# Kernel optimization log

Measured on AMD Instinct MI355X. Metric: run time of the kernel, lower is better.

Reference implementation:

```python
import jax, jax.numpy as jnp
import numpy as np

B, C, H, W = 512, 128, 16, 16
WS, HALO, HEADS = 16, 4, 4
HD = C // HEADS            # 32
SCALE = HD ** -0.5
WSH = WS + 2 * HALO        # 24 (padded window size)


def setup_inputs() -> dict:
    key = jax.random.key(0)
    ks = jax.random.split(key, 5)
    return {
        "x": jax.random.normal(ks[0], (B, C, H, W), dtype=jnp.float32),
        "qkv_w": jax.random.normal(ks[1], (3 * C, C), dtype=jnp.float32) * 0.02,
        "qkv_b": jax.random.normal(ks[2], (3 * C,), dtype=jnp.float32) * 0.02,
        "proj_w": jax.random.normal(ks[3], (C, C), dtype=jnp.float32) * 0.02,
        "proj_b": jax.random.normal(ks[4], (C,), dtype=jnp.float32) * 0.02,
    }


def reference(x, qkv_w, qkv_b, proj_w, proj_b):
    b, c, h, w = x.shape
    # reflect pad spatial dims by HALO
    xp = jnp.pad(x, ((0, 0), (0, 0), (HALO, HALO), (HALO, HALO)), mode="reflect")
    hp, wp = h + 2 * HALO, w + 2 * HALO
    # window partition on BHWC with window size WSH (non-overlapping, as in source)
    xw = xp.transpose(0, 2, 3, 1)  # [B, Hp, Wp, C]
    nh, nw = hp // WSH, wp // WSH
    xw = xw.reshape(b, nh, WSH, nw, WSH, c).transpose(0, 1, 3, 2, 4, 5)
    xw = xw.reshape(-1, WSH * WSH, c)  # [nW, 576, C]
    # QKV
    qkv = xw @ qkv_w.T + qkv_b  # [nW, 576, 3C]
    qkv = qkv.reshape(-1, WSH * WSH, 3, HEADS, HD).transpose(2, 0, 3, 1, 4)
    q, k, v = qkv[0], qkv[1], qkv[2]  # [nW, heads, 576, HD]
    # center query slice (contiguous flat slice, faithful to source)
    cs = HALO * WSH + HALO
    csz = WS * WS
    qc = jax.lax.dynamic_slice_in_dim(q, cs, csz, axis=2)  # [nW, heads, 256, HD]
    attn = jax.nn.softmax(jnp.einsum("whqd,whkd->whqk", qc, k) * SCALE, axis=-1)
    out = jnp.einsum("whqk,whkd->wqhd", attn, v).reshape(-1, csz, c)
    out = out @ proj_w.T + proj_b  # [nW, 256, C]
    # window reverse with window size WS over original H, W
    out = out.reshape(b, h // WS, w // WS, WS, WS, c).transpose(0, 1, 3, 2, 4, 5)
    out = out.reshape(b, h, w, c)
    return out.transpose(0, 3, 1, 2)  # [B, C, H, W]
```

## Files before the change

kernel.cpp:

```cpp
#include <hip/hip_runtime.h>
#include <hip/hip_bf16.h>
#include <stdint.h>


typedef short bf16x8 __attribute__((ext_vector_type(8)));
typedef float f32x4 __attribute__((ext_vector_type(4)));

__device__ __forceinline__ unsigned short f2bf(float f) {
  unsigned int u = __builtin_bit_cast(unsigned int, f);
  u += 0x7fffu + ((u >> 16) & 1u);
  return (unsigned short)(u >> 16);
}

__device__ __forceinline__ unsigned int cvt_pk_bf16(float lo, float hi) {
  unsigned int r;
  asm("v_cvt_pk_bf16_f32 %0, %1, %2" : "=v"(r) : "v"(lo), "v"(hi));
  return r;
}

__device__ __forceinline__ f32x4 mfma_16x16x32(bf16x8 a, bf16x8 b, f32x4 c) {
  return __builtin_amdgcn_mfma_f32_16x16x32_bf16(a, b, c, 0, 0, 0);
}

__device__ __forceinline__ void bar_lds() {
  asm volatile("s_waitcnt lgkmcnt(0)\n\ts_barrier" ::: "memory");
}

__global__ void wcvt(const float* __restrict__ proj_w, unsigned short* __restrict__ wp) {
  int i = blockIdx.x * 256 + threadIdx.x;
  if (i < 16384) wp[i] = f2bf(proj_w[i]);
}

__global__ __launch_bounds__(256, 2) void qkv_kernel(
    const float* __restrict__ x, const float* __restrict__ qkv_w,
    const float* __restrict__ qkv_b, unsigned short* __restrict__ qc,
    unsigned short* __restrict__ kw, unsigned short* __restrict__ vw) {
  __shared__ __align__(16) unsigned int XS[256 * 64];
  __shared__ __align__(16) unsigned short OB[64 * 128];
  const int b = blockIdx.x;
  const int tid = threadIdx.x;
  const int lane = tid & 63;
  const int wid = tid >> 6;
  const int g = lane >> 4;
  const int r16 = lane & 15;

  const float* xb = x + (size_t)b * 32768;

  bf16x8 wfr[6][4];
  float bias[6];
  #pragma unroll
  for (int i = 0; i < 6; ++i) {
    int nt_abs = wid + 4 * i;
    int n = nt_abs * 16 + r16;
    bias[i] = qkv_b[n];
    #pragma unroll
    for (int kt = 0; kt < 4; ++kt) {
      const float* wsrc = qkv_w + n * 128 + kt * 32 + g * 8;
      float4 w0 = *(const float4*)wsrc;
      float4 w1 = *(const float4*)(wsrc + 4);
      bf16x8 f;
      f[0] = (short)f2bf(w0.x); f[1] = (short)f2bf(w0.y);
      f[2] = (short)f2bf(w0.z); f[3] = (short)f2bf(w0.w);
      f[4] = (short)f2bf(w1.x); f[5] = (short)f2bf(w1.y);
      f[6] = (short)f2bf(w1.z); f[7] = (short)f2bf(w1.w);
      wfr[i][kt] = f;
    }
  }

  #pragma unroll 4
  for (int it = 0; it < 64; ++it) {
    float f0 = xb[(2 * it) * 256 + tid];
    float f1 = xb[(2 * it + 1) * 256 + tid];
    unsigned int pk = (unsigned int)f2bf(f0) | ((unsigned int)f2bf(f1) << 16);
    XS[tid * 64 + (it ^ ((tid & 7) << 2))] = pk;
  }
  bar_lds();

  for (int tile = 0; tile < 9; ++tile) {
    int sv[4];
    #pragma unroll
    for (int mt = 0; mt < 4; ++mt) {
      int tg = tile * 64 + mt * 16 + r16;
      int ph = tg / 24;
      int pw = tg - ph * 24;
      int hh = ph - 4; hh = (hh < 0) ? -hh : ((hh > 15) ? 30 - hh : hh);
      int wc = pw - 4; wc = (wc < 0) ? -wc : ((wc > 15) ? 30 - wc : wc);
      sv[mt] = hh * 16 + wc;
    }

    f32x4 acc[6][4];
    #pragma unroll
    for (int i = 0; i < 6; ++i)
      #pragma unroll
      for (int mt = 0; mt < 4; ++mt) acc[i][mt] = f32x4{0.f, 0.f, 0.f, 0.f};

    #pragma unroll
    for (int kt = 0; kt < 4; ++kt) {
      bf16x8 afr[4];
      #pragma unroll
      for (int mt = 0; mt < 4; ++mt)
        afr[mt] = __builtin_bit_cast(
            bf16x8, *(const uint4*)&XS[sv[mt] * 64 + ((kt * 16 + g * 4) ^ ((sv[mt] & 7) << 2))]);
      #pragma unroll
      for (int i = 0; i < 6; ++i)
        #pragma unroll
        for (int mt = 0; mt < 4; ++mt)
          acc[i][mt] = mfma_16x16x32(afr[mt], wfr[i][kt], acc[i][mt]);
    }

    #pragma unroll
    for (int sel = 0; sel < 3; ++sel) {
      bar_lds();
      #pragma unroll
      for (int j = 0; j < 2; ++j) {
        const int i = sel * 2 + j;
        int dcol = (wid + 4 * j) * 16 + r16;
        #pragma unroll
        for (int mt = 0; mt < 4; ++mt)
          #pragma unroll
          for (int rr = 0; rr < 4; ++rr)
            OB[(mt * 16 + 4 * g + rr) * 128 + dcol] = f2bf(acc[i][mt][rr] + bias[i]);
      }
      bar_lds();
      #pragma unroll
      for (int it = 0; it < 4; ++it) {
        int flat = it * 2048 + tid * 8;
        int tokl = flat >> 7, d0 = flat & 127;
        int tg = tile * 64 + tokl;
        uint4 val = *(const uint4*)&OB[tokl * 128 + d0];
        if (sel == 0) {
          int qi = tg - 100;
          if ((unsigned)qi < 256u)
            *(uint4*)(qc + ((size_t)b * 256 + qi) * 128 + d0) = val;
        } else if (sel == 1) {
          *(uint4*)(kw + ((size_t)b * 576 + tg) * 128 + d0) = val;
        } else {
          *(uint4*)(vw + ((size_t)b * 576 + tg) * 128 + d0) = val;
        }
      }
    }
  }
}

__global__ __launch_bounds__(256) void attn_kernel(
    const unsigned short* __restrict__ qc, const unsigned short* __restrict__ kw,
    const unsigned short* __restrict__ vw, unsigned short* __restrict__ ao) {
  __shared__ __align__(16) unsigned int KF[4 * 192 * 4];
  __shared__ __align__(16) unsigned short VT[32 * 200];
  const int bh = blockIdx.x;
  const int tid = threadIdx.x;
  const int lane = tid & 63;
  const int wid = tid >> 6;
  const int g = lane >> 4;
  const int r16 = lane & 15;
  const int qb = wid * 64;
  const int b = bh >> 2, h = bh & 3;

  const unsigned short* qcb = qc + (size_t)b * 256 * 128 + h * 32;
  const unsigned short* kb = kw + (size_t)b * 576 * 128 + h * 32;
  const unsigned short* vb = vw + (size_t)b * 576 * 128 + h * 32;

  unsigned int kreg[12], vreg[12];
  {
    const unsigned int* ks = (const unsigned int*)kb;
    const unsigned int* vs = (const unsigned int*)vb;
    #pragma unroll
    for (int it = 0; it < 12; ++it) {
      int f = it * 256 + tid;
      int kv = f >> 4, cu = f & 15;
      kreg[it] = ks[kv * 64 + cu];
      vreg[it] = vs[kv * 64 + cu];
    }
  }

  bf16x8 qf[4];
  #pragma unroll
  for (int qnt = 0; qnt < 4; ++qnt)
    qf[qnt] = __builtin_bit_cast(bf16x8, *(const uint4*)(qcb + (size_t)(qb + qnt * 16 + r16) * 128 + g * 8));

  float ls[4];
  #pragma unroll
  for (int i = 0; i < 4; ++i) ls[i] = 0.f;
  f32x4 oa[2][4];
  #pragma unroll
  for (int i = 0; i < 2; ++i)
    #pragma unroll
    for (int j = 0; j < 4; ++j) oa[i][j] = f32x4{0.f, 0.f, 0.f, 0.f};

  const float KE = 0.17677669529663687f * 1.4426950408889634f;

  for (int ch = 0; ch < 3; ++ch) {
    if (ch) bar_lds();
    #pragma unroll
    for (int it = 0; it < 12; ++it) {
      int f = it * 256 + tid;
      int kv = f >> 4, cu = f & 15;
      KF[(cu >> 2) * 768 + kv * 4 + (cu & 3)] = kreg[it];
      int kv32 = kv & 31;
      int idx = (kv >> 5) * 32 + ((kv32 & 15) >> 2) * 8 + (kv32 >> 4) * 4 + (kv32 & 3);
      unsigned int pk = vreg[it];
      VT[(2 * cu) * 200 + idx] = (unsigned short)(pk & 0xffffu);
      VT[(2 * cu + 1) * 200 + idx] = (unsigned short)(pk >> 16);
    }
    bar_lds();
    if (ch < 2) {
      const unsigned int* ks = (const unsigned int*)(kb + (size_t)(ch + 1) * 192 * 128);
      const unsigned int* vs = (const unsigned int*)(vb + (size_t)(ch + 1) * 192 * 128);
      #pragma unroll
      for (int it = 0; it < 12; ++it) {
        int f = it * 256 + tid;
        int kv = f >> 4, cu = f & 15;
        kreg[it] = ks[kv * 64 + cu];
        vreg[it] = vs[kv * 64 + cu];
      }
    }

    for (int kvt2 = 0; kvt2 < 6; ++kvt2) {
      bf16x8 kf0 = __builtin_bit_cast(bf16x8, *(const uint4*)&KF[g * 768 + (kvt2 * 32 + r16) * 4]);
      bf16x8 kf1 = __builtin_bit_cast(bf16x8, *(const uint4*)&KF[g * 768 + (kvt2 * 32 + 16 + r16) * 4]);
      f32x4 zero = f32x4{0.f, 0.f, 0.f, 0.f};
      f32x4 st0[4], st1[4];
      #pragma unroll
      for (int qnt = 0; qnt < 4; ++qnt) {
        st0[qnt] = mfma_16x16x32(kf0, qf[qnt], zero);
        st1[qnt] = mfma_16x16x32(kf1, qf[qnt], zero);
      }

      bf16x8 pf[4];
      #pragma unroll
      for (int qnt = 0; qnt < 4; ++qnt) {
        f32x4 s0 = st0[qnt], s1 = st1[qnt];
        float p[8];
        #pragma unroll
        for (int j = 0; j < 4; ++j) p[j] = __builtin_amdgcn_exp2f(s0[j] * KE);
        #pragma unroll
        for (int j = 0; j < 4; ++j) p[4 + j] = __builtin_amdgcn_exp2f(s1[j] * KE);
        float ts = ((p[0] + p[1]) + (p[2] + p[3])) + ((p[4] + p[5]) + (p[6] + p[7]));
        ls[qnt] += ts;
        uint4 pk4;
        pk4.x = cvt_pk_bf16(p[0], p[1]);
        pk4.y = cvt_pk_bf16(p[2], p[3]);
        pk4.z = cvt_pk_bf16(p[4], p[5]);
        pk4.w = cvt_pk_bf16(p[6], p[7]);
        pf[qnt] = __builtin_bit_cast(bf16x8, pk4);
      }
      #pragma unroll
      for (int dmt = 0; dmt < 2; ++dmt) {
        int d = dmt * 16 + r16;
        bf16x8 vf = __builtin_bit_cast(bf16x8, *(const uint4*)&VT[d * 200 + kvt2 * 32 + g * 8]);
        #pragma unroll
        for (int qnt = 0; qnt < 4; ++qnt)
          oa[dmt][qnt] = mfma_16x16x32(vf, pf[qnt], oa[dmt][qnt]);
      }
    }
  }

  #pragma unroll
  for (int qnt = 0; qnt < 4; ++qnt) {
    float l = ls[qnt];
    l += __shfl_xor(l, 16);
    l += __shfl_xor(l, 32);
    float rl = 1.0f / l;
    int q = qb + qnt * 16 + r16;
    #pragma unroll
    for (int dmt = 0; dmt < 2; ++dmt) {
      #pragma unroll
      for (int rr = 0; rr < 4; ++rr) {
        int d = dmt * 16 + 4 * g + rr;
        ao[((size_t)b * 256 + q) * 128 + h * 32 + d] = f2bf(oa[dmt][qnt][rr] * rl);
      }
    }
  }
}

__global__ __launch_bounds__(256) void proj_kernel(
    const unsigned short* __restrict__ ao, const unsigned short* __restrict__ wp,
    const float* __restrict__ proj_b, float* __restrict__ out) {
  __shared__ __align__(16) unsigned int A32[64 * 64];
  const int wg = blockIdx.x;
  const int b = wg >> 2;
  const int mq = wg & 3;
  const int tid = threadIdx.x;
  const int lane = tid & 63;
  const int wid = tid >> 6;
  const int g = lane >> 4;
  const int r16 = lane & 15;

  const unsigned int* asrc = (const unsigned int*)(ao + ((size_t)b * 256 + mq * 64) * 128);
  #pragma unroll
  for (int it = 0; it < 4; ++it) {
    int f = it * 256 + tid;
    int row = f >> 4, q4 = f & 15;
    uint4 v = *(const uint4*)&asrc[row * 64 + q4 * 4];
    *(uint4*)&A32[row * 64 + ((q4 * 4) ^ ((row & 7) << 2))] = v;
  }
  bar_lds();

  f32x4 acc[2][4];
  #pragma unroll
  for (int nt = 0; nt < 2; ++nt)
    #pragma unroll
    for (int mt = 0; mt < 4; ++mt) acc[nt][mt] = f32x4{0.f, 0.f, 0.f, 0.f};

  for (int kt = 0; kt < 4; ++kt) {
    bf16x8 afr[4];
    #pragma unroll
    for (int mt = 0; mt < 4; ++mt) {
      int row = mt * 16 + r16;
      int cub = (kt * 16 + g * 4) ^ ((row & 7) << 2);
      afr[mt] = __builtin_bit_cast(bf16x8, *(const uint4*)&A32[row * 64 + cub]);
    }
    #pragma unroll
    for (int nt = 0; nt < 2; ++nt) {
      int n = wid * 32 + nt * 16 + r16;
      bf16x8 bfr = __builtin_bit_cast(bf16x8, *(const uint4*)(wp + n * 128 + kt * 32 + g * 8));
      #pragma unroll
      for (int mt = 0; mt < 4; ++mt)
        acc[nt][mt] = mfma_16x16x32(afr[mt], bfr, acc[nt][mt]);
    }
  }

  #pragma unroll
  for (int nt = 0; nt < 2; ++nt) {
    int c = wid * 32 + nt * 16 + r16;
    float bv = proj_b[c];
    #pragma unroll
    for (int mt = 0; mt < 4; ++mt) {
      int t0 = mq * 64 + mt * 16 + 4 * g;
      float4 o;
      o.x = acc[nt][mt][0] + bv;
      o.y = acc[nt][mt][1] + bv;
      o.z = acc[nt][mt][2] + bv;
      o.w = acc[nt][mt][3] + bv;
      *(float4*)&out[((size_t)b * 128 + c) * 256 + t0] = o;
    }
  }
}

extern "C" void kernel_launch(void* const* d_in, const int* in_sizes, int n_in,
                              void* d_out, int out_size, void* d_ws, size_t ws_size,
                              hipStream_t stream) {
  const float* x = (const float*)d_in[0];
  const float* qkv_w = (const float*)d_in[1];
  const float* qkv_b = (const float*)d_in[2];
  const float* proj_w = (const float*)d_in[3];
  const float* proj_b = (const float*)d_in[4];
  float* out = (float*)d_out;

  unsigned short* ws16 = (unsigned short*)d_ws;
  unsigned short* wp = ws16;
  unsigned short* qcp = ws16 + 16384;
  unsigned short* kp = qcp + (size_t)16777216;
  unsigned short* vp = kp + (size_t)37748736;
  unsigned short* ap = vp + (size_t)37748736;

  hipLaunchKernelGGL(wcvt, dim3(64), dim3(256), 0, stream, proj_w, wp);
  hipLaunchKernelGGL(qkv_kernel, dim3(512), dim3(256), 0, stream, x, qkv_w, qkv_b, qcp, kp, vp);
  hipLaunchKernelGGL(attn_kernel, dim3(2048), dim3(256), 0, stream, qcp, kp, vp, ap);
  hipLaunchKernelGGL(proj_kernel, dim3(2048), dim3(256), 0, stream, ap, wp, proj_b, out);
}
```

Baseline: 224.1 us.

## Split QKV into transpose kernel plus per-tile grid with pre-converted weights

```diff
diff --git a/kernel.cpp b/kernel.cpp
--- a/kernel.cpp
+++ b/kernel.cpp
@@ -26,117 +26,123 @@
   asm volatile("s_waitcnt lgkmcnt(0)\n\ts_barrier" ::: "memory");
 }
 
-__global__ void wcvt(const float* __restrict__ proj_w, unsigned short* __restrict__ wp) {
+__device__ __forceinline__ int reflect_s(int tg) {
+  int ph = tg / 24;
+  int pw = tg - ph * 24;
+  int hh = ph - 4; hh = (hh < 0) ? -hh : ((hh > 15) ? 30 - hh : hh);
+  int wc = pw - 4; wc = (wc < 0) ? -wc : ((wc > 15) ? 30 - wc : wc);
+  return hh * 16 + wc;
+}
+
+__global__ void wcvt(const float* __restrict__ qkv_w, const float* __restrict__ proj_w,
+                     unsigned short* __restrict__ wq, unsigned short* __restrict__ wp) {
   int i = blockIdx.x * 256 + threadIdx.x;
+  if (i < 49152) wq[i] = f2bf(qkv_w[i]);
   if (i < 16384) wp[i] = f2bf(proj_w[i]);
 }
 
-__global__ __launch_bounds__(256, 2) void qkv_kernel(
-    const float* __restrict__ x, const float* __restrict__ qkv_w,
+__global__ __launch_bounds__(256) void xt_kernel(const float* __restrict__ x,
+                                                 unsigned short* __restrict__ xt) {
+  __shared__ __align__(16) unsigned int XS[256 * 64];
+  const int b = blockIdx.x, tid = threadIdx.x;
+  const float* xb = x + (size_t)b * 32768;
+  #pragma unroll 4
+  for (int it = 0; it < 64; ++it) {
+    float f0 = xb[(2 * it) * 256 + tid];
+    float f1 = xb[(2 * it + 1) * 256 + tid];
+    XS[tid * 64 + (it ^ ((tid & 7) << 2))] =
+        (unsigned int)f2bf(f0) | ((unsigned int)f2bf(f1) << 16);
+  }
+  bar_lds();
+  unsigned int* xtd = (unsigned int*)xt + (size_t)b * 16384;
+  #pragma unroll
+  for (int it = 0; it < 4; ++it) {
+    int s = it * 64 + (tid >> 2);
+    int cg = (tid & 3) * 4;
+    #pragma unroll
+    for (int m = 0; m < 4; ++m) {
+      uint4 v = *(const uint4*)&XS[s * 64 + (((cg + m) ^ (s & 7)) << 2)];
+      *(uint4*)&xtd[s * 64 + (cg + m) * 4] = v;
+    }
+  }
+}
+
+__global__ __launch_bounds__(256) void qkv_kernel(
+    const unsigned short* __restrict__ xt, const unsigned short* __restrict__ wq,
     const float* __restrict__ qkv_b, unsigned short* __restrict__ qc,
     unsigned short* __restrict__ kw, unsigned short* __restrict__ vw) {
-  __shared__ __align__(16) unsigned int XS[256 * 64];
   __shared__ __align__(16) unsigned short OB[64 * 128];
-  const int b = blockIdx.x;
+  const int bid = blockIdx.x;
+  const int logical = (bid & 7) * 576 + (bid >> 3);
+  const int b = logical / 9;
+  const int tile = logical - b * 9;
   const int tid = threadIdx.x;
   const int lane = tid & 63;
   const int wid = tid >> 6;
   const int g = lane >> 4;
   const int r16 = lane & 15;
 
-  const float* xb = x + (size_t)b * 32768;
-
-  bf16x8 wfr[6][4];
+  const unsigned int* xtd = (const unsigned int*)xt + (size_t)b * 16384;
+
+  int sv[4];
+  #pragma unroll
+  for (int mt = 0; mt < 4; ++mt)
+    sv[mt] = reflect_s(tile * 64 + mt * 16 + r16);
+
   float bias[6];
   #pragma unroll
-  for (int i = 0; i < 6; ++i) {
-    int nt_abs = wid + 4 * i;
-    int n = nt_abs * 16 + r16;
-    bias[i] = qkv_b[n];
-    #pragma unroll
-    for (int kt = 0; kt < 4; ++kt) {
-      const float* wsrc = qkv_w + n * 128 + kt * 32 + g * 8;
-      float4 w0 = *(const float4*)wsrc;
-      float4 w1 = *(const float4*)(wsrc + 4);
-      bf16x8 f;
-      f[0] = (short)f2bf(w0.x); f[1] = (short)f2bf(w0.y);
-      f[2] = (short)f2bf(w0.z); f[3] = (short)f2bf(w0.w);
-      f[4] = (short)f2bf(w1.x); f[5] = (short)f2bf(w1.y);
-      f[6] = (short)f2bf(w1.z); f[7] = (short)f2bf(w1.w);
-      wfr[i][kt] = f;
-    }
-  }
-
-  #pragma unroll 4
-  for (int it = 0; it < 64; ++it) {
-    float f0 = xb[(2 * it) * 256 + tid];
-    float f1 = xb[(2 * it + 1) * 256 + tid];
-    unsigned int pk = (unsigned int)f2bf(f0) | ((unsigned int)f2bf(f1) << 16);
-    XS[tid * 64 + (it ^ ((tid & 7) << 2))] = pk;
-  }
-  bar_lds();
-
-  for (int tile = 0; tile < 9; ++tile) {
-    int sv[4];
-    #pragma unroll
-    for (int mt = 0; mt < 4; ++mt) {
-      int tg = tile * 64 + mt * 16 + r16;
-      int ph = tg / 24;
-      int pw = tg - ph * 24;
-      int hh = ph - 4; hh = (hh < 0) ? -hh : ((hh > 15) ? 30 - hh : hh);
-      int wc = pw - 4; wc = (wc < 0) ? -wc : ((wc > 15) ? 30 - wc : wc);
-      sv[mt] = hh * 16 + wc;
-    }
-
-    f32x4 acc[6][4];
-    #pragma unroll
-    for (int i = 0; i < 6; ++i)
-      #pragma unroll
-      for (int mt = 0; mt < 4; ++mt) acc[i][mt] = f32x4{0.f, 0.f, 0.f, 0.f};
-
-    #pragma unroll
-    for (int kt = 0; kt < 4; ++kt) {
-      bf16x8 afr[4];
+  for (int i = 0; i < 6; ++i) bias[i] = qkv_b[(wid + 4 * i) * 16 + r16];
+
+  f32x4 acc[6][4];
+  #pragma unroll
+  for (int i = 0; i < 6; ++i)
+    #pragma unroll
+    for (int mt = 0; mt < 4; ++mt) acc[i][mt] = f32x4{0.f, 0.f, 0.f, 0.f};
+
+  #pragma unroll
+  for (int kt = 0; kt < 4; ++kt) {
+    bf16x8 afr[4];
+    #pragma unroll
+    for (int mt = 0; mt < 4; ++mt)
+      afr[mt] = __builtin_bit_cast(bf16x8, *(const uint4*)&xtd[sv[mt] * 64 + kt * 16 + g * 4]);
+    #pragma unroll
+    for (int i = 0; i < 6; ++i) {
+      int n = (wid + 4 * i) * 16 + r16;
+      bf16x8 bfr = __builtin_bit_cast(bf16x8, *(const uint4*)(wq + n * 128 + kt * 32 + g * 8));
       #pragma unroll
       for (int mt = 0; mt < 4; ++mt)
-        afr[mt] = __builtin_bit_cast(
-            bf16x8, *(const uint4*)&XS[sv[mt] * 64 + ((kt * 16 + g * 4) ^ ((sv[mt] & 7) << 2))]);
-      #pragma unroll
-      for (int i = 0; i < 6; ++i)
+        acc[i][mt] = mfma_16x16x32(afr[mt], bfr, acc[i][mt]);
+    }
+  }
+
+  #pragma unroll
+  for (int sel = 0; sel < 3; ++sel) {
+    bar_lds();
+    #pragma unroll
+    for (int j = 0; j < 2; ++j) {
+      const int i = sel * 2 + j;
+      int dcol = (wid + 4 * j) * 16 + r16;
+      #pragma unroll
+      for (int mt = 0; mt < 4; ++mt)
         #pragma unroll
-        for (int mt = 0; mt < 4; ++mt)
-          acc[i][mt] = mfma_16x16x32(afr[mt], wfr[i][kt], acc[i][mt]);
-    }
-
-    #pragma unroll
-    for (int sel = 0; sel < 3; ++sel) {
-      bar_lds();
-      #pragma unroll
-      for (int j = 0; j < 2; ++j) {
-        const int i = sel * 2 + j;
-        int dcol = (wid + 4 * j) * 16 + r16;
-        #pragma unroll
-        for (int mt = 0; mt < 4; ++mt)
-          #pragma unroll
-          for (int rr = 0; rr < 4; ++rr)
-            OB[(mt * 16 + 4 * g + rr) * 128 + dcol] = f2bf(acc[i][mt][rr] + bias[i]);
-      }
-      bar_lds();
-      #pragma unroll
-      for (int it = 0; it < 4; ++it) {
-        int flat = it * 2048 + tid * 8;
-        int tokl = flat >> 7, d0 = flat & 127;
-        int tg = tile * 64 + tokl;
-        uint4 val = *(const uint4*)&OB[tokl * 128 + d0];
-        if (sel == 0) {
-          int qi = tg - 100;
-          if ((unsigned)qi < 256u)
-            *(uint4*)(qc + ((size_t)b * 256 + qi) * 128 + d0) = val;
-        } else if (sel == 1) {
-          *(uint4*)(kw + ((size_t)b * 576 + tg) * 128 + d0) = val;
-        } else {
-          *(uint4*)(vw + ((size_t)b * 576 + tg) * 128 + d0) = val;
-        }
+        for (int rr = 0; rr < 4; ++rr)
+          OB[(mt * 16 + 4 * g + rr) * 128 + dcol] = f2bf(acc[i][mt][rr] + bias[i]);
+    }
+    bar_lds();
+    #pragma unroll
+    for (int it = 0; it < 4; ++it) {
+      int flat = it * 2048 + tid * 8;
+      int tokl = flat >> 7, d0 = flat & 127;
+      int tg = tile * 64 + tokl;
+      uint4 val = *(const uint4*)&OB[tokl * 128 + d0];
+      if (sel == 0) {
+        int qi = tg - 100;
+        if ((unsigned)qi < 256u)
+          *(uint4*)(qc + ((size_t)b * 256 + qi) * 128 + d0) = val;
+      } else if (sel == 1) {
+        *(uint4*)(kw + ((size_t)b * 576 + tg) * 128 + d0) = val;
+      } else {
+        *(uint4*)(vw + ((size_t)b * 576 + tg) * 128 + d0) = val;
       }
     }
   }
@@ -349,13 +355,16 @@
 
   unsigned short* ws16 = (unsigned short*)d_ws;
   unsigned short* wp = ws16;
-  unsigned short* qcp = ws16 + 16384;
+  unsigned short* wq = ws16 + 16384;
+  unsigned short* xtp = ws16 + 65536;
+  unsigned short* qcp = xtp + (size_t)16777216;
   unsigned short* kp = qcp + (size_t)16777216;
   unsigned short* vp = kp + (size_t)37748736;
-  unsigned short* ap = vp + (size_t)37748736;
-
-  hipLaunchKernelGGL(wcvt, dim3(64), dim3(256), 0, stream, proj_w, wp);
-  hipLaunchKernelGGL(qkv_kernel, dim3(512), dim3(256), 0, stream, x, qkv_w, qkv_b, qcp, kp, vp);
+  unsigned short* ap = xtp;
+
+  hipLaunchKernelGGL(wcvt, dim3(192), dim3(256), 0, stream, qkv_w, proj_w, wq, wp);
+  hipLaunchKernelGGL(xt_kernel, dim3(512), dim3(256), 0, stream, x, xtp);
+  hipLaunchKernelGGL(qkv_kernel, dim3(4608), dim3(256), 0, stream, xtp, wq, qkv_b, qcp, kp, vp);
   hipLaunchKernelGGL(attn_kernel, dim3(2048), dim3(256), 0, stream, qcp, kp, vp, ap);
   hipLaunchKernelGGL(proj_kernel, dim3(2048), dim3(256), 0, stream, ap, wp, proj_b, out);
 }
```

New measurement: 260.4 us. 1.16x slower.
